# Performance work log

Hardware: AMD Instinct MI355X
Metric: run time of the kernel (lower is better)

## Reference

```python
import jax, jax.numpy as jnp
import numpy as np

TEMPERATURE = 0.07
EPS = 1e-12  # F.normalize eps


def setup_inputs() -> dict:
    key = jax.random.key(0)
    k1, k2, k3 = jax.random.split(key, 3)
    B, D, N_CLASSES = 4096, 256, 1000
    return {
        "z_i": jax.random.normal(k1, (B, D), dtype=jnp.float32),
        "z_j": jax.random.normal(k2, (B, D), dtype=jnp.float32),
        "labels": jax.random.randint(k3, (B,), 0, N_CLASSES, dtype=jnp.int64),
    }


def _l2_normalize(x):
    norm = jnp.sqrt(jnp.sum(x * x, axis=1, keepdims=True))
    return x / jnp.maximum(norm, EPS)


def reference(z_i, z_j, labels):
    zi = _l2_normalize(z_i)
    zj = _l2_normalize(z_j)
    z = jnp.concatenate([zi, zj], axis=0)          # (2B, D)
    lab = jnp.concatenate([labels, labels], axis=0)  # (2B,)
    N = z.shape[0]

    sim = jnp.matmul(z, z.T) / TEMPERATURE          # (2B, 2B)

    eye = jnp.eye(N, dtype=bool)
    same = lab[:, None] == lab[None, :]
    pos_mask = same & ~eye                          # positives: same label, not self
    neg_mask = ~same                                # negatives: different label

    # pos_sim_i = sum of similarities over positives (a sum, per original code)
    pos_sim = jnp.sum(jnp.where(pos_mask, sim, 0.0), axis=1)  # (2B,)
    # log(neg_sim_i) = logsumexp over negatives (stable, same math as sum of exp)
    lse_neg = jax.nn.logsumexp(jnp.where(neg_mask, sim, -jnp.inf), axis=1)
    # -log(exp(p) / (exp(p) + n)) = log(1 + exp(log n - p))
    loss_i = jnp.logaddexp(0.0, lse_neg - pos_sim)  # (2B,)

    has_pos = jnp.any(pos_mask, axis=1)
    loss = jnp.sum(jnp.where(has_pos, loss_i, 0.0)) / N
    return loss
```

## Files before the change

### kernel.cpp

```cpp
#include <hip/hip_runtime.h>

#define NROWS 8192
#define BQ    4096
#define DDIM  256
#define INV_T (1.0f/0.07f)
#define K2EXP (1.4426950408889634f/0.07f)

typedef short bf16x8 __attribute__((ext_vector_type(8)));
typedef float f32x4  __attribute__((ext_vector_type(4)));
typedef unsigned short u16;

__device__ __forceinline__ u16 f2bf(float f) {
  unsigned u = __float_as_uint(f);
  u += 0x7fffu + ((u >> 16) & 1u);
  return (u16)(u >> 16);
}

__global__ void norm_cast_kernel(const float* __restrict__ zi,
                                 const float* __restrict__ zj,
                                 u16* __restrict__ zb) {
  int wave = threadIdx.x >> 6;
  int lane = threadIdx.x & 63;
  int row  = blockIdx.x * 4 + wave;
  const float* src = (row < BQ) ? (zi + (size_t)row * DDIM)
                                : (zj + (size_t)(row - BQ) * DDIM);
  float4 v = ((const float4*)src)[lane];
  float s = v.x*v.x + v.y*v.y + v.z*v.z + v.w*v.w;
  #pragma unroll
  for (int m = 32; m; m >>= 1) s += __shfl_xor(s, m, 64);
  float scale = 1.0f / fmaxf(sqrtf(s), 1e-12f);
  ushort4 o;
  o.x = f2bf(v.x * scale); o.y = f2bf(v.y * scale);
  o.z = f2bf(v.z * scale); o.w = f2bf(v.w * scale);
  ((ushort4*)(zb + (size_t)row * DDIM))[lane] = o;
}

#define GL2LDS(gp, lp) \
  __builtin_amdgcn_global_load_lds((__attribute__((address_space(1))) void*)(gp), \
                                   (__attribute__((address_space(3))) void*)(lp), 16, 0, 0)

__global__ __launch_bounds__(256) void simloss_kernel(
    const u16* __restrict__ zb, const int* __restrict__ labels,
    float* __restrict__ pos_p, float* __restrict__ neg_p) {
  __shared__ __align__(16) u16 lsA[128 * 32];
  __shared__ __align__(16) u16 lsB[128 * 32];

  const int tid  = threadIdx.x;
  const int w    = tid >> 6;
  const int lane = tid & 63;
  const int ln   = lane & 15;
  const int qd   = lane >> 4;
  const int wr   = w >> 1;
  const int wc   = w & 1;
  const int r0   = blockIdx.x * 128;
  const int cb   = blockIdx.y * 1024;

  const int strow = lane >> 2;
  const int stk   = (lane & 3) * 8;

  int rowidx[16], rowlab[16];
  #pragma unroll
  for (int ri = 0; ri < 4; ++ri)
    #pragma unroll
    for (int r = 0; r < 4; ++r) {
      int slot = ri * 4 + r;
      int row  = r0 + wr * 64 + ri * 16 + qd * 4 + r;
      rowidx[slot] = row;
      rowlab[slot] = labels[row & (BQ - 1)];
    }

  float posA[16], negA[16];
  #pragma unroll
  for (int i = 0; i < 16; ++i) { posA[i] = 0.0f; negA[i] = 0.0f; }

  for (int ci = 0; ci < 8; ++ci) {
    const int c0 = cb + ci * 128;
    int colv[4], clab[4];
    #pragma unroll
    for (int mi = 0; mi < 4; ++mi) {
      colv[mi] = c0 + wc * 64 + mi * 16 + ln;
      clab[mi] = labels[colv[mi] & (BQ - 1)];
    }

    const f32x4 z4 = {0.f, 0.f, 0.f, 0.f};
    f32x4 acc[4][4];
    #pragma unroll
    for (int ri = 0; ri < 4; ++ri)
      #pragma unroll
      for (int mi = 0; mi < 4; ++mi) acc[ri][mi] = z4;

    for (int kk = 0; kk < 8; ++kk) {
      const int k0 = kk * 32;
      #pragma unroll
      for (int j = 0; j < 2; ++j) {
        int rbase = w * 32 + j * 16;
        const u16* ga = zb + (size_t)(r0 + rbase + strow) * DDIM + k0 + stk;
        GL2LDS(ga, &lsA[rbase * 32]);
        const u16* gb = zb + (size_t)(c0 + rbase + strow) * DDIM + k0 + stk;
        GL2LDS(gb, &lsB[rbase * 32]);
      }
      __syncthreads();

      bf16x8 av[4], bv[4];
      #pragma unroll
      for (int ri = 0; ri < 4; ++ri)
        av[ri] = *(const bf16x8*)&lsA[(wr * 64 + ri * 16 + ln) * 32 + qd * 8];
      #pragma unroll
      for (int mi = 0; mi < 4; ++mi)
        bv[mi] = *(const bf16x8*)&lsB[(wc * 64 + mi * 16 + ln) * 32 + qd * 8];
      #pragma unroll
      for (int ri = 0; ri < 4; ++ri)
        #pragma unroll
        for (int mi = 0; mi < 4; ++mi)
          acc[ri][mi] = __builtin_amdgcn_mfma_f32_16x16x32_bf16(
              av[ri], bv[mi], acc[ri][mi], 0, 0, 0);
      __syncthreads();
    }

    #pragma unroll
    for (int ri = 0; ri < 4; ++ri)
      #pragma unroll
      for (int mi = 0; mi < 4; ++mi) {
        f32x4 v = acc[ri][mi];
        #pragma unroll
        for (int r = 0; r < 4; ++r) {
          int slot = ri * 4 + r;
          float s = v[r];
          bool same = (rowlab[slot] == clab[mi]);
          bool diag = (rowidx[slot] == colv[mi]);
          posA[slot] += (same && !diag) ? s : 0.0f;
          negA[slot] += same ? 0.0f : __builtin_amdgcn_exp2f(s * K2EXP);
        }
      }
  }

  #pragma unroll
  for (int i = 0; i < 16; ++i) {
    #pragma unroll
    for (int m = 1; m < 16; m <<= 1) {
      posA[i] += __shfl_xor(posA[i], m, 64);
      negA[i] += __shfl_xor(negA[i], m, 64);
    }
  }
  if (ln == 0) {
    int s = blockIdx.y * 2 + wc;
    #pragma unroll
    for (int i = 0; i < 16; ++i) {
      pos_p[(size_t)s * NROWS + rowidx[i]] = posA[i];
      neg_p[(size_t)s * NROWS + rowidx[i]] = negA[i];
    }
  }
}

__global__ void loss_kernel(const float* __restrict__ pos_p,
                            const float* __restrict__ neg_p,
                            float* __restrict__ out) {
  int t = threadIdx.x;
  float lsum = 0.0f;
  for (int rr = 0; rr < 8; ++rr) {
    int row = rr * 1024 + t;
    float p = 0.0f, n = 0.0f;
    #pragma unroll
    for (int s = 0; s < 16; ++s) {
      p += pos_p[(size_t)s * NROWS + row];
      n += neg_p[(size_t)s * NROWS + row];
    }
    p *= INV_T;
    lsum += log1pf(expf(logf(n) - p));
  }
  #pragma unroll
  for (int m = 32; m; m >>= 1) lsum += __shfl_xor(lsum, m, 64);
  __shared__ float red[16];
  if ((t & 63) == 0) red[t >> 6] = lsum;
  __syncthreads();
  if (t == 0) {
    float tot = 0.0f;
    #pragma unroll
    for (int i = 0; i < 16; ++i) tot += red[i];
    out[0] = tot * (1.0f / NROWS);
  }
}

extern "C" void kernel_launch(void* const* d_in, const int* in_sizes, int n_in,
                              void* d_out, int out_size, void* d_ws, size_t ws_size,
                              hipStream_t stream) {
  const float* zi     = (const float*)d_in[0];
  const float* zj     = (const float*)d_in[1];
  const int*   labels = (const int*)d_in[2];
  float*       out    = (float*)d_out;

  char* w = (char*)d_ws;
  u16*   zb    = (u16*)w;
  float* pos_p = (float*)(w + (size_t)NROWS * DDIM * sizeof(u16));
  float* neg_p = pos_p + 16 * NROWS;

  hipLaunchKernelGGL(norm_cast_kernel, dim3(2048), dim3(256), 0, stream, zi, zj, zb);
  hipLaunchKernelGGL(simloss_kernel, dim3(64, 8), dim3(256), 0, stream,
                     zb, labels, pos_p, neg_p);
  hipLaunchKernelGGL(loss_kernel, dim3(1), dim3(1024), 0, stream,
                     pos_p, neg_p, out);
}
```

Baseline: 130.0 us.

## Double simloss grid, swizzle LDS, reduce partials in-block, parallelize loss kernel

Halves the column range per block so the similarity kernel launches 1024 blocks instead of 512, and adds an occupancy hint to launch bounds. Applies an XOR swizzle to the LDS load and read addresses to reduce bank conflicts. The two column-half wave partials are combined through shared memory before one coalesced store per row, which keeps the same 16 partial slices. The final loss kernel now runs on 32 blocks with an atomicAdd into an output zeroed by a memset, replacing a single-block loop; the cost is an extra memset and the atomic's ordering nondeterminism.

```diff
diff --git a/kernel.cpp b/kernel.cpp
--- a/kernel.cpp
+++ b/kernel.cpp
@@ -39,7 +39,7 @@
   __builtin_amdgcn_global_load_lds((__attribute__((address_space(1))) void*)(gp), \
                                    (__attribute__((address_space(3))) void*)(lp), 16, 0, 0)
 
-__global__ __launch_bounds__(256) void simloss_kernel(
+__global__ __launch_bounds__(256, 4) void simloss_kernel(
     const u16* __restrict__ zb, const int* __restrict__ labels,
     float* __restrict__ pos_p, float* __restrict__ neg_p) {
   __shared__ __align__(16) u16 lsA[128 * 32];
@@ -53,27 +53,29 @@
   const int wr   = w >> 1;
   const int wc   = w & 1;
   const int r0   = blockIdx.x * 128;
-  const int cb   = blockIdx.y * 1024;
+  const int cb   = blockIdx.y * 512;
 
   const int strow = lane >> 2;
-  const int stk   = (lane & 3) * 8;
+  const int slot  = lane & 3;
+  const int stk   = (slot ^ ((strow >> 1) & 3)) * 8;
+  const int rdsw  = (ln >> 1) & 3;
 
   int rowidx[16], rowlab[16];
   #pragma unroll
   for (int ri = 0; ri < 4; ++ri)
     #pragma unroll
     for (int r = 0; r < 4; ++r) {
-      int slot = ri * 4 + r;
-      int row  = r0 + wr * 64 + ri * 16 + qd * 4 + r;
-      rowidx[slot] = row;
-      rowlab[slot] = labels[row & (BQ - 1)];
+      int slt = ri * 4 + r;
+      int row = r0 + wr * 64 + ri * 16 + qd * 4 + r;
+      rowidx[slt] = row;
+      rowlab[slt] = labels[row & (BQ - 1)];
     }
 
   float posA[16], negA[16];
   #pragma unroll
   for (int i = 0; i < 16; ++i) { posA[i] = 0.0f; negA[i] = 0.0f; }
 
-  for (int ci = 0; ci < 8; ++ci) {
+  for (int ci = 0; ci < 4; ++ci) {
     const int c0 = cb + ci * 128;
     int colv[4], clab[4];
     #pragma unroll
@@ -104,10 +106,10 @@
       bf16x8 av[4], bv[4];
       #pragma unroll
       for (int ri = 0; ri < 4; ++ri)
-        av[ri] = *(const bf16x8*)&lsA[(wr * 64 + ri * 16 + ln) * 32 + qd * 8];
+        av[ri] = *(const bf16x8*)&lsA[(wr * 64 + ri * 16 + ln) * 32 + (qd ^ rdsw) * 8];
       #pragma unroll
       for (int mi = 0; mi < 4; ++mi)
-        bv[mi] = *(const bf16x8*)&lsB[(wc * 64 + mi * 16 + ln) * 32 + qd * 8];
+        bv[mi] = *(const bf16x8*)&lsB[(wc * 64 + mi * 16 + ln) * 32 + (qd ^ rdsw) * 8];
       #pragma unroll
       for (int ri = 0; ri < 4; ++ri)
         #pragma unroll
@@ -124,12 +126,12 @@
         f32x4 v = acc[ri][mi];
         #pragma unroll
         for (int r = 0; r < 4; ++r) {
-          int slot = ri * 4 + r;
+          int slt = ri * 4 + r;
           float s = v[r];
-          bool same = (rowlab[slot] == clab[mi]);
-          bool diag = (rowidx[slot] == colv[mi]);
-          posA[slot] += (same && !diag) ? s : 0.0f;
-          negA[slot] += same ? 0.0f : __builtin_amdgcn_exp2f(s * K2EXP);
+          bool same = (rowlab[slt] == clab[mi]);
+          bool diag = (rowidx[slt] == colv[mi]);
+          posA[slt] += (same && !diag) ? s : 0.0f;
+          negA[slt] += same ? 0.0f : __builtin_amdgcn_exp2f(s * K2EXP);
         }
       }
   }
@@ -142,42 +144,46 @@
       negA[i] += __shfl_xor(negA[i], m, 64);
     }
   }
+
+  __syncthreads();
+  float* scp = (float*)lsA;
+  float* scn = (float*)lsB;
   if (ln == 0) {
-    int s = blockIdx.y * 2 + wc;
     #pragma unroll
     for (int i = 0; i < 16; ++i) {
-      pos_p[(size_t)s * NROWS + rowidx[i]] = posA[i];
-      neg_p[(size_t)s * NROWS + rowidx[i]] = negA[i];
-    }
+      int lr = rowidx[i] - r0;
+      scp[wc * 128 + lr] = posA[i];
+      scn[wc * 128 + lr] = negA[i];
+    }
+  }
+  __syncthreads();
+  if (tid < 128) {
+    float p = scp[tid] + scp[128 + tid];
+    float n = scn[tid] + scn[128 + tid];
+    pos_p[(size_t)blockIdx.y * NROWS + r0 + tid] = p;
+    neg_p[(size_t)blockIdx.y * NROWS + r0 + tid] = n;
   }
 }
 
 __global__ void loss_kernel(const float* __restrict__ pos_p,
                             const float* __restrict__ neg_p,
                             float* __restrict__ out) {
-  int t = threadIdx.x;
-  float lsum = 0.0f;
-  for (int rr = 0; rr < 8; ++rr) {
-    int row = rr * 1024 + t;
-    float p = 0.0f, n = 0.0f;
-    #pragma unroll
-    for (int s = 0; s < 16; ++s) {
-      p += pos_p[(size_t)s * NROWS + row];
-      n += neg_p[(size_t)s * NROWS + row];
-    }
-    p *= INV_T;
-    lsum += log1pf(expf(logf(n) - p));
-  }
-  #pragma unroll
-  for (int m = 32; m; m >>= 1) lsum += __shfl_xor(lsum, m, 64);
-  __shared__ float red[16];
-  if ((t & 63) == 0) red[t >> 6] = lsum;
+  int row = blockIdx.x * 256 + threadIdx.x;
+  float p = 0.0f, n = 0.0f;
+  #pragma unroll
+  for (int s = 0; s < 16; ++s) {
+    p += pos_p[(size_t)s * NROWS + row];
+    n += neg_p[(size_t)s * NROWS + row];
+  }
+  float l = log1pf(expf(logf(n) - p * INV_T));
+  #pragma unroll
+  for (int m = 32; m; m >>= 1) l += __shfl_xor(l, m, 64);
+  __shared__ float red[4];
+  if ((threadIdx.x & 63) == 0) red[threadIdx.x >> 6] = l;
   __syncthreads();
-  if (t == 0) {
-    float tot = 0.0f;
-    #pragma unroll
-    for (int i = 0; i < 16; ++i) tot += red[i];
-    out[0] = tot * (1.0f / NROWS);
+  if (threadIdx.x == 0) {
+    float tot = red[0] + red[1] + red[2] + red[3];
+    atomicAdd(out, tot * (1.0f / NROWS));
   }
 }
 
@@ -194,9 +200,10 @@
   float* pos_p = (float*)(w + (size_t)NROWS * DDIM * sizeof(u16));
   float* neg_p = pos_p + 16 * NROWS;
 
+  hipMemsetAsync(out, 0, sizeof(float), stream);
   hipLaunchKernelGGL(norm_cast_kernel, dim3(2048), dim3(256), 0, stream, zi, zj, zb);
-  hipLaunchKernelGGL(simloss_kernel, dim3(64, 8), dim3(256), 0, stream,
+  hipLaunchKernelGGL(simloss_kernel, dim3(64, 16), dim3(256), 0, stream,
                      zb, labels, pos_p, neg_p);
-  hipLaunchKernelGGL(loss_kernel, dim3(1), dim3(1024), 0, stream,
+  hipLaunchKernelGGL(loss_kernel, dim3(32), dim3(256), 0, stream,
                      pos_p, neg_p, out);
 }
```

New measurement: 220.7 us. 69.8% more time.
